# Kernel tuning notes

Hardware: AMD Instinct MI355X
Metric: run time of the kernel (lower is better)

## Reference

```python
import jax, jax.numpy as jnp
import numpy as np

N_NODES = 100000
N_EDGES = 1000000
IN_DIM = 64
HID = 64
OUT_DIM = 32
NUM_GRAPHS = 512


def setup_inputs() -> dict:
    key = jax.random.key(0)
    ks = jax.random.split(key, 16)
    x = jax.random.normal(ks[0], (N_NODES, IN_DIM), dtype=jnp.float32)
    edge_index = jax.random.randint(ks[1], (2, N_EDGES), 0, N_NODES, dtype=jnp.int64)
    batch = jnp.sort(jax.random.randint(ks[2], (N_NODES,), 0, NUM_GRAPHS, dtype=jnp.int64))

    def lin(k, i, o):
        s = 1.0 / np.sqrt(i)
        kw, kb = jax.random.split(k)
        return (jax.random.uniform(kw, (i, o), jnp.float32, -s, s),
                jax.random.uniform(kb, (o,), jnp.float32, -s, s))

    W1a, b1a = lin(ks[3], IN_DIM, HID)
    W2a, b2a = lin(ks[4], HID, HID)
    W1b, b1b = lin(ks[5], HID, HID)
    W2b, b2b = lin(ks[6], HID, HID)
    Wp1, bp1 = lin(ks[7], HID, HID)
    Wp2, bp2 = lin(ks[8], HID, OUT_DIM)
    return dict(x=x, edge_index=edge_index, batch=batch,
                W1a=W1a, b1a=b1a, W2a=W2a, b2a=b2a,
                W1b=W1b, b1b=b1b, W2b=W2b, b2b=b2b,
                Wp1=Wp1, bp1=bp1, Wp2=Wp2, bp2=bp2)


def _gin_layer(x, edge_index, W1, b1, W2, b2):
    # GINConv (eps=0): h_i = MLP(x_i + sum_{j->i} x_j)
    src, dst = edge_index[0], edge_index[1]
    agg = jax.ops.segment_sum(x[src], dst, num_segments=N_NODES)  # [N, d]
    h = x + agg
    h = jnp.maximum(h @ W1 + b1, 0.0) @ W2 + b2
    return h


def reference(x, edge_index, batch,
              W1a, b1a, W2a, b2a,
              W1b, b1b, W2b, b2b,
              Wp1, bp1, Wp2, bp2):
    # layer 0 (dropout is identity in eval mode)
    x = _gin_layer(x, edge_index, W1a, b1a, W2a, b2a)
    x = jnp.maximum(x, 0.0)
    # layer 1
    x = _gin_layer(x, edge_index, W1b, b1b, W2b, b2b)
    emb = x  # pre-ReLU embedding of last executed conv
    x = jnp.maximum(x, 0.0)
    # global mean pool over graphs
    sums = jax.ops.segment_sum(x, batch, num_segments=NUM_GRAPHS)  # [G, d]
    cnts = jax.ops.segment_sum(jnp.ones((x.shape[0],), x.dtype), batch, num_segments=NUM_GRAPHS)
    pooled = sums / jnp.maximum(cnts, 1.0)[:, None]
    # post-MLP (dropout identity in eval)
    out = (pooled @ Wp1 + bp1) @ Wp2 + bp2
    return emb, jax.nn.log_softmax(out, axis=1)
```

## Files before the change

### kernel.cpp

```cpp
#include <hip/hip_runtime.h>
#include <math.h>

#define N_NODES 100000
#define N_EDGES 1000000
#define HID 64
#define OUT_DIM 32
#define NUM_GRAPHS 512
#define CAP 48
#define NBUCK 98
#define BCAP 11264
#define ACHUNK 4096

typedef __attribute__((ext_vector_type(4))) float f4v;
typedef __attribute__((ext_vector_type(4))) int i4v;
typedef __attribute__((ext_vector_type(8))) short s8v;
typedef __attribute__((ext_vector_type(4))) short s4vs;

static __device__ inline short f2bf(float f) {
  unsigned u = __float_as_uint(f);
  unsigned r = (u + 0x7fffu + ((u >> 16) & 1u)) >> 16;
  return (short)r;
}
static __device__ inline float bf2f(short s) {
  return __uint_as_float(((unsigned)(unsigned short)s) << 16);
}

__global__ __launch_bounds__(256) void bucket_prep_kernel(
    const int* __restrict__ ei, int* __restrict__ bedge,
    int* __restrict__ bcnt, int n_edges,
    const float* __restrict__ W1a, const float* __restrict__ W2a,
    const float* __restrict__ W1b, const float* __restrict__ W2b,
    short* __restrict__ wtab, const int* __restrict__ batch,
    int* __restrict__ starts) {
  int nEB = (n_edges + ACHUNK - 1) / ACHUNK;
  int tid = threadIdx.x;

  if ((int)blockIdx.x >= nEB) {
    int t = ((int)blockIdx.x - nEB) * 256 + tid;
    if (t < 16384) {
      int which = t >> 12;
      int r = t & 4095;
      const float* W = (which == 0) ? W1a : (which == 1) ? W2a : (which == 2) ? W1b : W2b;
      short* hiT = wtab + which * 8192;
      short* loT = hiT + 4096;
      int n = r & 63, k = r >> 6;
      float w = W[k * HID + n];
      short h = f2bf(w);
      hiT[n * HID + k] = h;
      loT[n * HID + k] = f2bf(w - bf2f(h));
    } else if (t < 16384 + NUM_GRAPHS + 1) {
      int g = t - 16384;
      int lo = 0, hi = N_NODES;
      while (lo < hi) {
        int mid = (lo + hi) >> 1;
        if (batch[mid] < g) lo = mid + 1; else hi = mid;
      }
      starts[g] = lo;
    }
    return;
  }

  __shared__ int s_pack[ACHUNK];
  __shared__ unsigned char s_b[ACHUNK];
  __shared__ int s_sorted[ACHUNK];
  __shared__ int s_hist[NBUCK];
  __shared__ int s_off[NBUCK];
  __shared__ int s_base[NBUCK];

  int e0 = blockIdx.x * ACHUNK;
  int n = n_edges - e0;
  if (n > ACHUNK) n = ACHUNK;

  for (int i = tid; i < NBUCK; i += 256) s_hist[i] = 0;
  __syncthreads();

  for (int i = tid; i < n; i += 256) {
    int src = ei[e0 + i];
    int dst = ei[n_edges + e0 + i];
    int b = dst >> 10;
    s_pack[i] = src | ((dst & 1023) << 17);
    s_b[i] = (unsigned char)b;
    atomicAdd(&s_hist[b], 1);
  }
  __syncthreads();

  if (tid < NBUCK) s_off[tid] = s_hist[tid];
  __syncthreads();
  for (int off = 1; off < NBUCK; off <<= 1) {
    int v = 0;
    if (tid < NBUCK && tid >= off) v = s_off[tid - off];
    __syncthreads();
    if (tid < NBUCK && tid >= off) s_off[tid] += v;
    __syncthreads();
  }
  if (tid < NBUCK) {
    int excl = s_off[tid] - s_hist[tid];
    s_off[tid] = excl;
    int c = s_hist[tid];
    s_base[tid] = c > 0 ? atomicAdd(&bcnt[tid], c) : 0;
  }
  __syncthreads();

  for (int i = tid; i < n; i += 256) {
    int p = atomicAdd(&s_off[s_b[i]], 1);
    s_sorted[p] = s_pack[i];
  }
  __syncthreads();

  int wv = tid >> 6;
  int lane = tid & 63;
  for (int b = wv; b < NBUCK; b += 4) {
    int cnt = s_hist[b];
    if (cnt == 0) continue;
    int start = s_off[b] - cnt;
    int gbase = s_base[b];
    for (int i = lane; i < cnt; i += 64) {
      int idx = gbase + i;
      if (idx < BCAP) bedge[b * BCAP + idx] = s_sorted[start + i];
    }
  }
}

__global__ __launch_bounds__(256) void csr_from_buckets_kernel(
    const int* __restrict__ bedge, const int* __restrict__ bcnt,
    int* __restrict__ deg, int* __restrict__ csr) {
  __shared__ int ldeg[1024];
  int b = blockIdx.x;
  int tid = threadIdx.x;
  for (int i = tid; i < 1024; i += 256) ldeg[i] = 0;
  __syncthreads();

  int n = bcnt[b];
  if (n > BCAP) n = BCAP;
  const int* bb = bedge + b * BCAP;
  for (int i0 = tid * 4; i0 < n; i0 += 1024) {
    int e0, e1, e2, e3;
    int rem = n - i0;
    if (rem >= 4) {
      i4v v = *(const i4v*)(bb + i0);
      e0 = v.x; e1 = v.y; e2 = v.z; e3 = v.w;
    } else {
      e0 = bb[i0];
      e1 = (rem > 1) ? bb[i0 + 1] : 0;
      e2 = (rem > 2) ? bb[i0 + 2] : 0;
      e3 = 0;
    }
    {
      int local = e0 >> 17, src = e0 & 0x1FFFF;
      int slot = atomicAdd(&ldeg[local], 1);
      if (slot < CAP) csr[(((size_t)b << 10) | local) * CAP + slot] = src;
    }
    if (n - i0 > 1) {
      int local = e1 >> 17, src = e1 & 0x1FFFF;
      int slot = atomicAdd(&ldeg[local], 1);
      if (slot < CAP) csr[(((size_t)b << 10) | local) * CAP + slot] = src;
    }
    if (n - i0 > 2) {
      int local = e2 >> 17, src = e2 & 0x1FFFF;
      int slot = atomicAdd(&ldeg[local], 1);
      if (slot < CAP) csr[(((size_t)b << 10) | local) * CAP + slot] = src;
    }
    if (n - i0 > 3) {
      int local = e3 >> 17, src = e3 & 0x1FFFF;
      int slot = atomicAdd(&ldeg[local], 1);
      if (slot < CAP) csr[(((size_t)b << 10) | local) * CAP + slot] = src;
    }
  }
  __syncthreads();

  for (int i = tid; i < 1024; i += 256) {
    int node = (b << 10) + i;
    if (node < N_NODES) deg[node] = ldeg[i];
  }
}

__global__ __launch_bounds__(256) void gather_kernel(
    const float* __restrict__ x, const int* __restrict__ deg,
    const int* __restrict__ csr, short* __restrict__ hbufHi,
    short* __restrict__ hbufLo, int n_nodes) {
  int lane = threadIdx.x & 63;
  int node = blockIdx.x * (blockDim.x >> 6) + (threadIdx.x >> 6);
  if (node >= n_nodes) return;
  int g = lane >> 4;
  int sub = lane & 15;

  const f4v* x4 = (const f4v*)x;
  f4v a0 = (g == 0) ? x4[(size_t)node * 16 + sub] : (f4v){0.f, 0.f, 0.f, 0.f};
  int idx = (lane < 16) ? csr[node * CAP + lane] : 0;
  int d = deg[node];
  if (d > CAP) d = CAP;

  f4v a1 = {0.f, 0.f, 0.f, 0.f};
  f4v a2 = {0.f, 0.f, 0.f, 0.f};
  f4v a3 = {0.f, 0.f, 0.f, 0.f};
  if (d > 0) {
    int j1 = g, j2 = 4 + g, j3 = 8 + g, j4 = 12 + g;
    int s1 = __shfl(idx, j1);
    int s2 = __shfl(idx, j2);
    int s3 = __shfl(idx, j3);
    int s4 = __shfl(idx, j4);
    if (j1 < d) a0 += x4[(size_t)s1 * 16 + sub];
    if (j2 < d) a1 += x4[(size_t)s2 * 16 + sub];
    if (j3 < d) a2 += x4[(size_t)s3 * 16 + sub];
    if (j4 < d) a3 += x4[(size_t)s4 * 16 + sub];
  }
  if (d > 16) {
    int idx2 = (lane < 32) ? csr[node * CAP + 16 + lane] : 0;
    for (int j0 = 16; j0 < d; j0 += 16) {
      int j1 = j0 + g, j2 = j0 + 4 + g, j3 = j0 + 8 + g, j4 = j0 + 12 + g;
      int s1 = __shfl(idx2, j1 - 16);
      int s2 = __shfl(idx2, j2 - 16);
      int s3 = __shfl(idx2, j3 - 16);
      int s4 = __shfl(idx2, j4 - 16);
      if (j1 < d) a0 += x4[(size_t)s1 * 16 + sub];
      if (j2 < d) a1 += x4[(size_t)s2 * 16 + sub];
      if (j3 < d) a2 += x4[(size_t)s3 * 16 + sub];
      if (j4 < d) a3 += x4[(size_t)s4 * 16 + sub];
    }
  }
  f4v a = (a0 + a1) + (a2 + a3);
  a.x += __shfl_xor(a.x, 16); a.y += __shfl_xor(a.y, 16);
  a.z += __shfl_xor(a.z, 16); a.w += __shfl_xor(a.w, 16);
  a.x += __shfl_xor(a.x, 32); a.y += __shfl_xor(a.y, 32);
  a.z += __shfl_xor(a.z, 32); a.w += __shfl_xor(a.w, 32);
  if (g == 0) {
    s4vs hi, lo;
#pragma unroll
    for (int c = 0; c < 4; c++) {
      float v = a[c];
      short hb = f2bf(v);
      hi[c] = hb;
      lo[c] = f2bf(v - bf2f(hb));
    }
    ((s4vs*)hbufHi)[(size_t)node * 16 + sub] = hi;
    ((s4vs*)hbufLo)[(size_t)node * 16 + sub] = lo;
  }
}

#define LPAD 72

__global__ __launch_bounds__(256) void gin_mlp_mfma_kernel(
    const short* __restrict__ hbufHi, const short* __restrict__ hbufLo,
    const short* __restrict__ W1hi, const short* __restrict__ W1lo,
    const float* __restrict__ b1,
    const short* __restrict__ W2hi, const short* __restrict__ W2lo,
    const float* __restrict__ b2,
    float* __restrict__ out, int n_nodes, int apply_relu) {
  __shared__ short lds[4][2][16 * LPAD];

  int lane = threadIdx.x & 63;
  int wv = threadIdx.x >> 6;
  int m = lane & 15;
  int quad = lane >> 4;
  int nodeBase = blockIdx.x * 64 + wv * 16;
  int node = nodeBase + m;
  bool valid = node < n_nodes;

  s8v ahi[2], alo[2];
#pragma unroll
  for (int kb = 0; kb < 2; kb++) {
    int off = node * HID + kb * 32 + quad * 8;
    if (valid) {
      ahi[kb] = *(const s8v*)(hbufHi + off);
      alo[kb] = *(const s8v*)(hbufLo + off);
    } else {
      ahi[kb] = (s8v){0, 0, 0, 0, 0, 0, 0, 0};
      alo[kb] = (s8v){0, 0, 0, 0, 0, 0, 0, 0};
    }
  }

  f4v acc[4];
#pragma unroll
  for (int nt = 0; nt < 4; nt++) acc[nt] = (f4v){0.f, 0.f, 0.f, 0.f};
#pragma unroll
  for (int kb = 0; kb < 2; kb++) {
#pragma unroll
    for (int nt = 0; nt < 4; nt++) {
      int n = nt * 16 + m;
      s8v bh = *(const s8v*)(W1hi + n * HID + kb * 32 + quad * 8);
      s8v bl = *(const s8v*)(W1lo + n * HID + kb * 32 + quad * 8);
      acc[nt] = __builtin_amdgcn_mfma_f32_16x16x32_bf16(ahi[kb], bh, acc[nt], 0, 0, 0);
      acc[nt] = __builtin_amdgcn_mfma_f32_16x16x32_bf16(ahi[kb], bl, acc[nt], 0, 0, 0);
      acc[nt] = __builtin_amdgcn_mfma_f32_16x16x32_bf16(alo[kb], bh, acc[nt], 0, 0, 0);
    }
  }

  short* Lhi = lds[wv][0];
  short* Llo = lds[wv][1];
#pragma unroll
  for (int nt = 0; nt < 4; nt++) {
    int col = nt * 16 + m;
    float bb = b1[col];
#pragma unroll
    for (int r = 0; r < 4; r++) {
      int row = quad * 4 + r;
      float h = fmaxf(acc[nt][r] + bb, 0.f);
      short hb = f2bf(h);
      Lhi[row * LPAD + col] = hb;
      Llo[row * LPAD + col] = f2bf(h - bf2f(hb));
    }
  }
  __syncthreads();

  s8v a2hi[2], a2lo[2];
#pragma unroll
  for (int kb = 0; kb < 2; kb++) {
    int off = m * LPAD + kb * 32 + quad * 8;
    a2hi[kb] = *(const s8v*)(Lhi + off);
    a2lo[kb] = *(const s8v*)(Llo + off);
  }

  f4v acc2[4];
#pragma unroll
  for (int nt = 0; nt < 4; nt++) acc2[nt] = (f4v){0.f, 0.f, 0.f, 0.f};
#pragma unroll
  for (int kb = 0; kb < 2; kb++) {
#pragma unroll
    for (int nt = 0; nt < 4; nt++) {
      int n = nt * 16 + m;
      s8v bh = *(const s8v*)(W2hi + n * HID + kb * 32 + quad * 8);
      s8v bl = *(const s8v*)(W2lo + n * HID + kb * 32 + quad * 8);
      acc2[nt] = __builtin_amdgcn_mfma_f32_16x16x32_bf16(a2hi[kb], bh, acc2[nt], 0, 0, 0);
      acc2[nt] = __builtin_amdgcn_mfma_f32_16x16x32_bf16(a2hi[kb], bl, acc2[nt], 0, 0, 0);
      acc2[nt] = __builtin_amdgcn_mfma_f32_16x16x32_bf16(a2lo[kb], bh, acc2[nt], 0, 0, 0);
    }
  }

#pragma unroll
  for (int nt = 0; nt < 4; nt++) {
    int col = nt * 16 + m;
    float bb = b2[col];
#pragma unroll
    for (int r = 0; r < 4; r++) {
      int row = quad * 4 + r;
      int onode = nodeBase + row;
      if (onode < n_nodes) {
        float o = acc2[nt][r] + bb;
        if (apply_relu) o = fmaxf(o, 0.f);
        out[(size_t)onode * HID + col] = o;
      }
    }
  }
}

__global__ __launch_bounds__(64) void poolhead_kernel(
    const float* __restrict__ emb, const int* __restrict__ starts,
    const float* __restrict__ Wp1, const float* __restrict__ bp1,
    const float* __restrict__ Wp2, const float* __restrict__ bp2,
    float* __restrict__ out) {
  int lane = threadIdx.x & 63;
  int g = blockIdx.x;
  int group = lane >> 4, sub = lane & 15;
  int s0 = starts[g], s1 = starts[g + 1];

  const f4v* e4 = (const f4v*)emb;
  f4v acc = {0.f, 0.f, 0.f, 0.f};
  for (int n = s0 + group; n < s1; n += 4) {
    f4v v = e4[(size_t)n * 16 + sub];
    v.x = fmaxf(v.x, 0.f); v.y = fmaxf(v.y, 0.f);
    v.z = fmaxf(v.z, 0.f); v.w = fmaxf(v.w, 0.f);
    acc += v;
  }
  acc.x += __shfl_xor(acc.x, 16); acc.y += __shfl_xor(acc.y, 16);
  acc.z += __shfl_xor(acc.z, 16); acc.w += __shfl_xor(acc.w, 16);
  acc.x += __shfl_xor(acc.x, 32); acc.y += __shfl_xor(acc.y, 32);
  acc.z += __shfl_xor(acc.z, 32); acc.w += __shfl_xor(acc.w, 32);
  int srcl = lane >> 2;
  float v0 = __shfl(acc.x, srcl);
  float v1 = __shfl(acc.y, srcl);
  float v2 = __shfl(acc.z, srcl);
  float v3 = __shfl(acc.w, srcl);
  int r = lane & 3;
  float psum = (r == 0) ? v0 : (r == 1) ? v1 : (r == 2) ? v2 : v3;

  float c = fmaxf((float)(s1 - s0), 1.0f);
  float p = psum / c;

  float t = bp1[lane];
#pragma unroll
  for (int k = 0; k < HID; k++) {
    t += __shfl(p, k) * Wp1[k * HID + lane];
  }

  float acc2 = 0.0f;
#pragma unroll
  for (int k = 0; k < HID; k++) {
    float tk = __shfl(t, k);
    if (lane < OUT_DIM) acc2 += tk * Wp2[k * OUT_DIM + lane];
  }
  float o = (lane < OUT_DIM) ? (acc2 + bp2[lane]) : -1e30f;

  float m = o;
#pragma unroll
  for (int off = 32; off >= 1; off >>= 1) m = fmaxf(m, __shfl_xor(m, off));
  float ex = (lane < OUT_DIM) ? expf(o - m) : 0.0f;
  float s = ex;
#pragma unroll
  for (int off = 32; off >= 1; off >>= 1) s += __shfl_xor(s, off);
  float lse = m + logf(s);
  if (lane < OUT_DIM) out[g * OUT_DIM + lane] = o - lse;
}

extern "C" void kernel_launch(void* const* d_in, const int* in_sizes, int n_in,
                              void* d_out, int out_size, void* d_ws, size_t ws_size,
                              hipStream_t stream) {
  const float* x   = (const float*)d_in[0];
  const int* ei    = (const int*)d_in[1];
  const int* batch = (const int*)d_in[2];
  const float* W1a = (const float*)d_in[3];
  const float* b1a = (const float*)d_in[4];
  const float* W2a = (const float*)d_in[5];
  const float* b2a = (const float*)d_in[6];
  const float* W1b = (const float*)d_in[7];
  const float* b1b = (const float*)d_in[8];
  const float* W2b = (const float*)d_in[9];
  const float* b2b = (const float*)d_in[10];
  const float* Wp1 = (const float*)d_in[11];
  const float* bp1 = (const float*)d_in[12];
  const float* Wp2 = (const float*)d_in[13];
  const float* bp2 = (const float*)d_in[14];

  float* emb    = (float*)d_out;
  float* logits = (float*)d_out + (size_t)N_NODES * HID;
  float* x1 = emb;

  short* hbufHi = (short*)d_ws;
  short* hbufLo = hbufHi + (size_t)N_NODES * HID;
  int* bedge   = (int*)d_ws;
  int* bcnt    = bedge + NBUCK * BCAP;
  int* deg     = (int*)((float*)d_ws + (size_t)N_NODES * HID);
  int* csr     = deg + N_NODES;
  int* starts  = csr + (size_t)N_NODES * CAP;
  short* wtab  = (short*)(starts + NUM_GRAPHS + 1);
  short* W1aHi = wtab + 0 * 4096; short* W1aLo = wtab + 1 * 4096;
  short* W2aHi = wtab + 2 * 4096; short* W2aLo = wtab + 3 * 4096;
  short* W1bHi = wtab + 4 * 4096; short* W1bLo = wtab + 5 * 4096;
  short* W2bHi = wtab + 6 * 4096; short* W2bLo = wtab + 7 * 4096;

  hipMemsetAsync(bcnt, 0, NBUCK * sizeof(int), stream);
  int nEB = (N_EDGES + ACHUNK - 1) / ACHUNK;
  int prepB = (16384 + NUM_GRAPHS + 1 + 255) / 256;
  bucket_prep_kernel<<<nEB + prepB, 256, 0, stream>>>(
      ei, bedge, bcnt, N_EDGES, W1a, W2a, W1b, W2b, wtab, batch, starts);

  csr_from_buckets_kernel<<<NBUCK, 256, 0, stream>>>(bedge, bcnt, deg, csr);

  int gather_blocks = (N_NODES + 3) / 4;
  int mlp_blocks = (N_NODES + 63) / 64;

  gather_kernel<<<gather_blocks, 256, 0, stream>>>(
      x, deg, csr, hbufHi, hbufLo, N_NODES);
  gin_mlp_mfma_kernel<<<mlp_blocks, 256, 0, stream>>>(
      hbufHi, hbufLo, W1aHi, W1aLo, b1a, W2aHi, W2aLo, b2a, x1, N_NODES, 1);

  gather_kernel<<<gather_blocks, 256, 0, stream>>>(
      x1, deg, csr, hbufHi, hbufLo, N_NODES);
  gin_mlp_mfma_kernel<<<mlp_blocks, 256, 0, stream>>>(
      hbufHi, hbufLo, W1bHi, W1bLo, b1b, W2bHi, W2bLo, b2b, emb, N_NODES, 0);

  poolhead_kernel<<<NUM_GRAPHS, 64, 0, stream>>>(
      emb, starts, Wp1, bp1, Wp2, bp2, logits);
}
```

Baseline: 318.2 us.

## Fuse mean-pool accumulation into final MLP kernel and widen prep/CSR blocks

Moves the global mean-pool sum out of the pool-head kernel and into the epilogue of the second MLP kernel. Each wave reduces its 16 rows and does atomic adds into a per-graph sum buffer that the prep kernel zeroes. This removes the re-read of the 25.6 MB embedding in the pool kernel. Separately, bucket prep uses 512-thread blocks with vectorized int4 edge loads, and the CSR build uses 1024-thread blocks. The cost is float atomic contention plus nondeterministic summation order.

Result: faster. 311.9 us (-2.0%).

```diff
diff --git a/kernel.cpp b/kernel.cpp
--- a/kernel.cpp
+++ b/kernel.cpp
@@ -25,18 +25,20 @@
   return __uint_as_float(((unsigned)(unsigned short)s) << 16);
 }
 
-__global__ __launch_bounds__(256) void bucket_prep_kernel(
+#define PREP_T (16384 + NUM_GRAPHS + 1 + NUM_GRAPHS * HID)
+
+__global__ __launch_bounds__(512) void bucket_prep_kernel(
     const int* __restrict__ ei, int* __restrict__ bedge,
     int* __restrict__ bcnt, int n_edges,
     const float* __restrict__ W1a, const float* __restrict__ W2a,
     const float* __restrict__ W1b, const float* __restrict__ W2b,
     short* __restrict__ wtab, const int* __restrict__ batch,
-    int* __restrict__ starts) {
+    int* __restrict__ starts, float* __restrict__ gsum) {
   int nEB = (n_edges + ACHUNK - 1) / ACHUNK;
   int tid = threadIdx.x;
 
   if ((int)blockIdx.x >= nEB) {
-    int t = ((int)blockIdx.x - nEB) * 256 + tid;
+    int t = ((int)blockIdx.x - nEB) * 512 + tid;
     if (t < 16384) {
       int which = t >> 12;
       int r = t & 4095;
@@ -56,6 +58,8 @@
         if (batch[mid] < g) lo = mid + 1; else hi = mid;
       }
       starts[g] = lo;
+    } else if (t < PREP_T) {
+      gsum[t - 16384 - NUM_GRAPHS - 1] = 0.0f;
     }
     return;
   }
@@ -71,16 +75,21 @@
   int n = n_edges - e0;
   if (n > ACHUNK) n = ACHUNK;
 
-  for (int i = tid; i < NBUCK; i += 256) s_hist[i] = 0;
-  __syncthreads();
-
-  for (int i = tid; i < n; i += 256) {
-    int src = ei[e0 + i];
-    int dst = ei[n_edges + e0 + i];
-    int b = dst >> 10;
-    s_pack[i] = src | ((dst & 1023) << 17);
-    s_b[i] = (unsigned char)b;
-    atomicAdd(&s_hist[b], 1);
+  for (int i = tid; i < NBUCK; i += 512) s_hist[i] = 0;
+  __syncthreads();
+
+  for (int i0 = tid * 4; i0 < n; i0 += 2048) {
+    i4v vs = *(const i4v*)(ei + e0 + i0);
+    i4v vd = *(const i4v*)(ei + n_edges + e0 + i0);
+#pragma unroll
+    for (int k = 0; k < 4; k++) {
+      int src = vs[k];
+      int dst = vd[k];
+      int b = dst >> 10;
+      s_pack[i0 + k] = src | ((dst & 1023) << 17);
+      s_b[i0 + k] = (unsigned char)b;
+      atomicAdd(&s_hist[b], 1);
+    }
   }
   __syncthreads();
 
@@ -101,7 +110,7 @@
   }
   __syncthreads();
 
-  for (int i = tid; i < n; i += 256) {
+  for (int i = tid; i < n; i += 512) {
     int p = atomicAdd(&s_off[s_b[i]], 1);
     s_sorted[p] = s_pack[i];
   }
@@ -109,7 +118,7 @@
 
   int wv = tid >> 6;
   int lane = tid & 63;
-  for (int b = wv; b < NBUCK; b += 4) {
+  for (int b = wv; b < NBUCK; b += 8) {
     int cnt = s_hist[b];
     if (cnt == 0) continue;
     int start = s_off[b] - cnt;
@@ -121,19 +130,19 @@
   }
 }
 
-__global__ __launch_bounds__(256) void csr_from_buckets_kernel(
+__global__ __launch_bounds__(1024) void csr_from_buckets_kernel(
     const int* __restrict__ bedge, const int* __restrict__ bcnt,
     int* __restrict__ deg, int* __restrict__ csr) {
   __shared__ int ldeg[1024];
   int b = blockIdx.x;
   int tid = threadIdx.x;
-  for (int i = tid; i < 1024; i += 256) ldeg[i] = 0;
+  ldeg[tid] = 0;
   __syncthreads();
 
   int n = bcnt[b];
   if (n > BCAP) n = BCAP;
   const int* bb = bedge + b * BCAP;
-  for (int i0 = tid * 4; i0 < n; i0 += 1024) {
+  for (int i0 = tid * 4; i0 < n; i0 += 4096) {
     int e0, e1, e2, e3;
     int rem = n - i0;
     if (rem >= 4) {
@@ -150,17 +159,17 @@
       int slot = atomicAdd(&ldeg[local], 1);
       if (slot < CAP) csr[(((size_t)b << 10) | local) * CAP + slot] = src;
     }
-    if (n - i0 > 1) {
+    if (rem > 1) {
       int local = e1 >> 17, src = e1 & 0x1FFFF;
       int slot = atomicAdd(&ldeg[local], 1);
       if (slot < CAP) csr[(((size_t)b << 10) | local) * CAP + slot] = src;
     }
-    if (n - i0 > 2) {
+    if (rem > 2) {
       int local = e2 >> 17, src = e2 & 0x1FFFF;
       int slot = atomicAdd(&ldeg[local], 1);
       if (slot < CAP) csr[(((size_t)b << 10) | local) * CAP + slot] = src;
     }
-    if (n - i0 > 3) {
+    if (rem > 3) {
       int local = e3 >> 17, src = e3 & 0x1FFFF;
       int slot = atomicAdd(&ldeg[local], 1);
       if (slot < CAP) csr[(((size_t)b << 10) | local) * CAP + slot] = src;
@@ -168,10 +177,8 @@
   }
   __syncthreads();
 
-  for (int i = tid; i < 1024; i += 256) {
-    int node = (b << 10) + i;
-    if (node < N_NODES) deg[node] = ldeg[i];
-  }
+  int node = (b << 10) + tid;
+  if (node < N_NODES) deg[node] = ldeg[tid];
 }
 
 __global__ __launch_bounds__(256) void gather_kernel(
@@ -245,7 +252,8 @@
     const float* __restrict__ b1,
     const short* __restrict__ W2hi, const short* __restrict__ W2lo,
     const float* __restrict__ b2,
-    float* __restrict__ out, int n_nodes, int apply_relu) {
+    float* __restrict__ out, int n_nodes, int apply_relu,
+    const int* __restrict__ batch, float* __restrict__ gsum, int do_pool) {
   __shared__ short lds[4][2][16 * LPAD];
 
   int lane = threadIdx.x & 63;
@@ -326,6 +334,7 @@
     }
   }
 
+  float po[4][4];
 #pragma unroll
   for (int nt = 0; nt < 4; nt++) {
     int col = nt * 16 + m;
@@ -334,47 +343,54 @@
     for (int r = 0; r < 4; r++) {
       int row = quad * 4 + r;
       int onode = nodeBase + row;
+      float o = acc2[nt][r] + bb;
+      po[nt][r] = 0.f;
       if (onode < n_nodes) {
-        float o = acc2[nt][r] + bb;
-        if (apply_relu) o = fmaxf(o, 0.f);
+        po[nt][r] = fmaxf(o, 0.f);
+        if (apply_relu) o = po[nt][r];
         out[(size_t)onode * HID + col] = o;
       }
     }
   }
+
+  if (do_pool) {
+    int nb = nodeBase < n_nodes ? nodeBase : n_nodes - 1;
+    int ne = nodeBase + 15 < n_nodes ? nodeBase + 15 : n_nodes - 1;
+    int gfirst = batch[nb];
+    int glast = batch[ne];
+    if (gfirst == glast) {
+#pragma unroll
+      for (int nt = 0; nt < 4; nt++) {
+        float v = (po[nt][0] + po[nt][1]) + (po[nt][2] + po[nt][3]);
+        v += __shfl_xor(v, 16);
+        v += __shfl_xor(v, 32);
+        if (quad == 0) atomicAdd(&gsum[gfirst * HID + nt * 16 + m], v);
+      }
+    } else {
+#pragma unroll
+      for (int nt = 0; nt < 4; nt++) {
+#pragma unroll
+        for (int r = 0; r < 4; r++) {
+          int onode = nodeBase + quad * 4 + r;
+          if (onode < n_nodes)
+            atomicAdd(&gsum[batch[onode] * HID + nt * 16 + m], po[nt][r]);
+        }
+      }
+    }
+  }
 }
 
 __global__ __launch_bounds__(64) void poolhead_kernel(
-    const float* __restrict__ emb, const int* __restrict__ starts,
+    const float* __restrict__ gsum, const int* __restrict__ starts,
     const float* __restrict__ Wp1, const float* __restrict__ bp1,
     const float* __restrict__ Wp2, const float* __restrict__ bp2,
     float* __restrict__ out) {
   int lane = threadIdx.x & 63;
   int g = blockIdx.x;
-  int group = lane >> 4, sub = lane & 15;
   int s0 = starts[g], s1 = starts[g + 1];
 
-  const f4v* e4 = (const f4v*)emb;
-  f4v acc = {0.f, 0.f, 0.f, 0.f};
-  for (int n = s0 + group; n < s1; n += 4) {
-    f4v v = e4[(size_t)n * 16 + sub];
-    v.x = fmaxf(v.x, 0.f); v.y = fmaxf(v.y, 0.f);
-    v.z = fmaxf(v.z, 0.f); v.w = fmaxf(v.w, 0.f);
-    acc += v;
-  }
-  acc.x += __shfl_xor(acc.x, 16); acc.y += __shfl_xor(acc.y, 16);
-  acc.z += __shfl_xor(acc.z, 16); acc.w += __shfl_xor(acc.w, 16);
-  acc.x += __shfl_xor(acc.x, 32); acc.y += __shfl_xor(acc.y, 32);
-  acc.z += __shfl_xor(acc.z, 32); acc.w += __shfl_xor(acc.w, 32);
-  int srcl = lane >> 2;
-  float v0 = __shfl(acc.x, srcl);
-  float v1 = __shfl(acc.y, srcl);
-  float v2 = __shfl(acc.z, srcl);
-  float v3 = __shfl(acc.w, srcl);
-  int r = lane & 3;
-  float psum = (r == 0) ? v0 : (r == 1) ? v1 : (r == 2) ? v2 : v3;
-
   float c = fmaxf((float)(s1 - s0), 1.0f);
-  float p = psum / c;
+  float p = gsum[g * HID + lane] / c;
 
   float t = bp1[lane];
 #pragma unroll
@@ -432,6 +448,7 @@
   int* csr     = deg + N_NODES;
   int* starts  = csr + (size_t)N_NODES * CAP;
   short* wtab  = (short*)(starts + NUM_GRAPHS + 1);
+  float* gsum  = (float*)(wtab + 8 * 4096);
   short* W1aHi = wtab + 0 * 4096; short* W1aLo = wtab + 1 * 4096;
   short* W2aHi = wtab + 2 * 4096; short* W2aLo = wtab + 3 * 4096;
   short* W1bHi = wtab + 4 * 4096; short* W1bLo = wtab + 5 * 4096;
@@ -439,11 +456,11 @@
 
   hipMemsetAsync(bcnt, 0, NBUCK * sizeof(int), stream);
   int nEB = (N_EDGES + ACHUNK - 1) / ACHUNK;
-  int prepB = (16384 + NUM_GRAPHS + 1 + 255) / 256;
-  bucket_prep_kernel<<<nEB + prepB, 256, 0, stream>>>(
-      ei, bedge, bcnt, N_EDGES, W1a, W2a, W1b, W2b, wtab, batch, starts);
-
-  csr_from_buckets_kernel<<<NBUCK, 256, 0, stream>>>(bedge, bcnt, deg, csr);
+  int prepB = (PREP_T + 511) / 512;
+  bucket_prep_kernel<<<nEB + prepB, 512, 0, stream>>>(
+      ei, bedge, bcnt, N_EDGES, W1a, W2a, W1b, W2b, wtab, batch, starts, gsum);
+
+  csr_from_buckets_kernel<<<NBUCK, 1024, 0, stream>>>(bedge, bcnt, deg, csr);
 
   int gather_blocks = (N_NODES + 3) / 4;
   int mlp_blocks = (N_NODES + 63) / 64;
@@ -451,13 +468,15 @@
   gather_kernel<<<gather_blocks, 256, 0, stream>>>(
       x, deg, csr, hbufHi, hbufLo, N_NODES);
   gin_mlp_mfma_kernel<<<mlp_blocks, 256, 0, stream>>>(
-      hbufHi, hbufLo, W1aHi, W1aLo, b1a, W2aHi, W2aLo, b2a, x1, N_NODES, 1);
+      hbufHi, hbufLo, W1aHi, W1aLo, b1a, W2aHi, W2aLo, b2a, x1, N_NODES,
+      1, batch, gsum, 0);
 
   gather_kernel<<<gather_blocks, 256, 0, stream>>>(
       x1, deg, csr, hbufHi, hbufLo, N_NODES);
   gin_mlp_mfma_kernel<<<mlp_blocks, 256, 0, stream>>>(
-      hbufHi, hbufLo, W1bHi, W1bLo, b1b, W2bHi, W2bLo, b2b, emb, N_NODES, 0);
+      hbufHi, hbufLo, W1bHi, W1bLo, b1b, W2bHi, W2bLo, b2b, emb, N_NODES,
+      0, batch, gsum, 1);
 
   poolhead_kernel<<<NUM_GRAPHS, 64, 0, stream>>>(
-      emb, starts, Wp1, bp1, Wp2, bp2, logits);
-}
+      gsum, starts, Wp1, bp1, Wp2, bp2, logits);
+}
```
